# Optimization experiments

Hardware: AMD Instinct MI355X
Metric: run time of the kernel (lower is better)

## Reference

```python
import jax, jax.numpy as jnp
import numpy as np

B, S, E = 2, 2048, 2048
H, KV, D = 16, 4, 128
G = H // KV  # query heads per kv head
THETA = 10000.0


def setup_inputs() -> dict:
    key = jax.random.key(0)
    ks = jax.random.split(key, 5)
    scale = 0.02
    return {
        "x": jax.random.normal(ks[0], (B, S, E), dtype=jnp.float32),
        "Wq": jax.random.normal(ks[1], (E, H * D), dtype=jnp.float32) * scale,
        "Wk": jax.random.normal(ks[2], (E, KV * D), dtype=jnp.float32) * scale,
        "Wv": jax.random.normal(ks[3], (E, KV * D), dtype=jnp.float32) * scale,
        "Wo": jax.random.normal(ks[4], (E, E), dtype=jnp.float32) * scale,
    }


def _rope_tables(seq_len, head_dim, theta):
    inv_freq = 1.0 / theta ** (jnp.arange(0, head_dim, 2, dtype=jnp.float32) / head_dim)
    t = jnp.arange(seq_len, dtype=jnp.float32)
    freqs = jnp.outer(t, inv_freq)  # [S, D/2]
    cos = jnp.concatenate([jnp.cos(freqs), jnp.cos(freqs)], axis=-1)  # [S, D]
    sin = jnp.concatenate([jnp.sin(freqs), jnp.sin(freqs)], axis=-1)
    return cos, sin


def _apply_rope(x, cos, sin):
    # x: [B, h, S, D]; cos/sin: [S, D] broadcast over batch/heads
    d2 = x.shape[-1] // 2
    x1, x2 = x[..., :d2], x[..., d2:]
    rotated = jnp.concatenate([-x2, x1], axis=-1)
    return x * cos + rotated * sin


def reference(x, Wq, Wk, Wv, Wo):
    b, s, _ = x.shape
    q = (x @ Wq).reshape(b, s, H, D).transpose(0, 2, 1, 3)   # [B,H,S,D]
    k = (x @ Wk).reshape(b, s, KV, D).transpose(0, 2, 1, 3)  # [B,KV,S,D]
    v = (x @ Wv).reshape(b, s, KV, D).transpose(0, 2, 1, 3)

    cos, sin = _rope_tables(s, D, THETA)
    q = _apply_rope(q, cos, sin)
    k = _apply_rope(k, cos, sin)

    # GQA: q head h attends to kv head h // G (repeat_interleave order)
    qg = q.reshape(b, KV, G, s, D)
    scores = jnp.einsum("bkgsd,bktd->bkgst", qg, k) / jnp.sqrt(jnp.asarray(D, x.dtype))
    causal = jnp.tril(jnp.ones((s, s), dtype=bool))
    scores = jnp.where(causal, scores, jnp.asarray(-jnp.inf, scores.dtype))
    attn = jax.nn.softmax(scores, axis=-1)
    out = jnp.einsum("bkgst,bktd->bkgsd", attn, v)  # [B,KV,G,S,D]
    out = out.reshape(b, H, s, D).transpose(0, 2, 1, 3).reshape(b, s, H * D)
    return out @ Wo
```

## Files before the change

### kernel.cpp

```cpp
#include <hip/hip_runtime.h>
#include <stdint.h>

#define B_ 2
#define S_ 2048
#define E_ 2048
#define H_ 16
#define KV_ 4
#define D_ 128
#define G_ (H_ / KV_)
#define M_ (B_ * S_)

typedef unsigned short u16;
typedef unsigned int u32;
typedef __bf16 bf16x8 __attribute__((ext_vector_type(8)));
typedef float f32x4 __attribute__((ext_vector_type(4)));

__device__ __forceinline__ u16 f2bf(float f) {
  __bf16 h = (__bf16)f;
  return *(u16*)&h;
}
__device__ __forceinline__ float bf2f(u16 x) {
  return __uint_as_float(((u32)x) << 16);
}
__device__ __forceinline__ void store_c(u16* p, float v) { *p = f2bf(v); }
__device__ __forceinline__ void store_c(float* p, float v) { *p = v; }

__device__ __forceinline__ void gload_lds16(const u16* g, u16* lds) {
  __builtin_amdgcn_global_load_lds((const __attribute__((address_space(1))) u32*)g,
                                   (__attribute__((address_space(3))) u32*)lds,
                                   16, 0, 0);
}

__global__ __launch_bounds__(256) void convert_fp32_bf16(const float4* __restrict__ x,
                                                         uint2* __restrict__ o, int n4) {
  int i = blockIdx.x * 256 + threadIdx.x;
  if (i >= n4) return;
  float4 v = x[i];
  uint2 r;
  r.x = (u32)f2bf(v.x) | ((u32)f2bf(v.y) << 16);
  r.y = (u32)f2bf(v.z) | ((u32)f2bf(v.w) << 16);
  o[i] = r;
}

__global__ __launch_bounds__(256) void transpose_conv_w(const float* __restrict__ W,
                                                        u16* __restrict__ Wt,
                                                        int Kdim, int Ndim) {
  __shared__ float tile[32][33];
  int n0 = blockIdx.x * 32, k0 = blockIdx.y * 32;
  int tx = threadIdx.x, ty = threadIdx.y;
#pragma unroll
  for (int i = 0; i < 4; i++) {
    int r = ty + i * 8;
    tile[r][tx] = W[(size_t)(k0 + r) * Ndim + n0 + tx];
  }
  __syncthreads();
#pragma unroll
  for (int i = 0; i < 4; i++) {
    int r = ty + i * 8;
    Wt[(size_t)(n0 + r) * Kdim + k0 + tx] = f2bf(tile[tx][r]);
  }
}

__global__ __launch_bounds__(256) void transpose_v(const u16* __restrict__ V,
                                                   u16* __restrict__ Vt) {
  __shared__ u16 tile[32][33];
  int bkv = blockIdx.z;
  int b = bkv / KV_, kv = bkv % KV_;
  int s0 = blockIdx.x * 32, d0 = blockIdx.y * 32;
  int tx = threadIdx.x, ty = threadIdx.y;
#pragma unroll
  for (int i = 0; i < 4; i++) {
    int r = ty + i * 8;
    tile[r][tx] = V[((size_t)((b * S_ + s0 + r) * KV_ + kv)) * D_ + d0 + tx];
  }
  __syncthreads();
#pragma unroll
  for (int i = 0; i < 4; i++) {
    int r = ty + i * 8;
    Vt[((size_t)(b * KV_ + kv) * D_ + d0 + r) * S_ + s0 + tx] = tile[tx][r];
  }
}

__global__ __launch_bounds__(256) void rope_k_repack(const u16* __restrict__ Kin,
                                                     u16* __restrict__ Kp, int total) {
  int idx = blockIdx.x * 256 + threadIdx.x;
  if (idx >= total) return;
  int d = idx & 63;
  int rem = idx >> 6;
  int kv = rem % KV_;
  int row = rem / KV_;
  int b = row >> 11;
  int spos = row & (S_ - 1);
  size_t src = ((size_t)row * KV_ + kv) * D_ + d;
  float x0 = bf2f(Kin[src]);
  float x1 = bf2f(Kin[src + 64]);
  float ang = (float)spos * expf(-0.14391156831212787f * (float)d);
  float sn, cs;
  sincosf(ang, &sn, &cs);
  size_t dst = ((size_t)((b * KV_ + kv) * S_ + spos)) * D_ + d;
  Kp[dst]      = f2bf(x0 * cs - x1 * sn);
  Kp[dst + 64] = f2bf(x1 * cs + x0 * sn);
}

__global__ __launch_bounds__(256) void rope_q_inplace(u16* __restrict__ Qb, int total) {
  int idx = blockIdx.x * 256 + threadIdx.x;
  if (idx >= total) return;
  int d = idx & 63;
  int rem = idx >> 6;
  int h = rem & (H_ - 1);
  int row = rem >> 4;
  int spos = row & (S_ - 1);
  size_t base = ((size_t)row * H_ + h) * D_ + d;
  float x0 = bf2f(Qb[base]);
  float x1 = bf2f(Qb[base + 64]);
  float ang = (float)spos * expf(-0.14391156831212787f * (float)d);
  float sn, cs;
  sincosf(ang, &sn, &cs);
  const float scale = 0.08838834764831845f;
  Qb[base]      = f2bf((x0 * cs - x1 * sn) * scale);
  Qb[base + 64] = f2bf((x1 * cs + x0 * sn) * scale);
}

template <typename CT>
__device__ __forceinline__ void gemm256_body(const u16* __restrict__ A,
                                             const u16* __restrict__ Bt,
                                             CT* __restrict__ C,
                                             int Kdim, int Ndim, int m0, int n0) {
  extern __shared__ __align__(16) u16 smem[];
  const int tid  = threadIdx.x;
  const int lane = tid & 63;
  const int wave = tid >> 6;
  const int wm   = wave >> 2;
  const int wn   = wave & 3;
  const int bh   = wn >> 1;
  const int nb   = (wn & 1) * 64;
  const int quad = lane >> 4, lm = lane & 15;

  int soff[2], sldb[2];
#pragma unroll
  for (int i = 0; i < 2; i++) {
    int cc  = i * 512 + tid;
    int row = cc >> 3;
    int q   = (cc & 7) ^ (row & 7);
    soff[i] = row * Kdim + q * 8;
    sldb[i] = (i * 512 + wave * 64) * 8;
  }
  auto STAGE = [&](const u16* g, u16* l) {
    gload_lds16(g + soff[0], l + sldb[0]);
    gload_lds16(g + soff[1], l + sldb[1]);
  };

  int cs0 = ((0 + quad) ^ (lm & 7)) * 8;
  int cs1 = ((4 + quad) ^ (lm & 7)) * 8;

  const u16* Ag = A  + (size_t)m0 * Kdim;
  const u16* Bg = Bt + (size_t)n0 * Kdim;
  const size_t hstep = (size_t)128 * Kdim;

  f32x4 acc[8][4];
  f32x4 zero = {0.f, 0.f, 0.f, 0.f};
#pragma unroll
  for (int m = 0; m < 8; m++)
#pragma unroll
    for (int n = 0; n < 4; n++) acc[m][n] = zero;

  const int NKT = Kdim >> 6;

  STAGE(Bg,             smem + 32768 + 0 * 8192);
  STAGE(Ag,             smem + 0 * 8192);
  STAGE(Ag + hstep,     smem + 1 * 8192);
  STAGE(Bg + hstep,     smem + 32768 + 1 * 8192);
  STAGE(Bg + 64,        smem + 32768 + 2 * 8192);
  STAGE(Ag + 64,        smem + 2 * 8192);
  STAGE(Ag + hstep + 64, smem + 3 * 8192);
  asm volatile("s_waitcnt vmcnt(6)" ::: "memory");
  __builtin_amdgcn_s_barrier();

  for (int kt = 0; kt < NKT; ++kt) {
    const int cur = kt & 1;
    const u16* regA = smem + (cur * 2 + wm) * 8192;
    const u16* regB = smem + 32768 + (cur * 2 + bh) * 8192;
    bf16x8 af[4][2], bf[4][2];

#pragma unroll
    for (int n = 0; n < 4; n++) {
      bf[n][0] = *(const bf16x8*)(regB + (nb + n * 16 + lm) * 64 + cs0);
      bf[n][1] = *(const bf16x8*)(regB + (nb + n * 16 + lm) * 64 + cs1);
    }
#pragma unroll
    for (int m = 0; m < 4; m++) {
      af[m][0] = *(const bf16x8*)(regA + (m * 16 + lm) * 64 + cs0);
      af[m][1] = *(const bf16x8*)(regA + (m * 16 + lm) * 64 + cs1);
    }
    if (kt + 1 < NKT)
      STAGE(Bg + hstep + (size_t)(kt + 1) * 64,
            smem + 32768 + (((kt + 1) & 1) * 2 + 1) * 8192);
    asm volatile("s_waitcnt lgkmcnt(0)" ::: "memory");
    __builtin_amdgcn_s_barrier();
    __builtin_amdgcn_s_setprio(1);
#pragma unroll
    for (int m = 0; m < 4; m++)
#pragma unroll
      for (int n = 0; n < 2; n++) {
        acc[m][n] = __builtin_amdgcn_mfma_f32_16x16x32_bf16(af[m][0], bf[n][0], acc[m][n], 0, 0, 0);
        acc[m][n] = __builtin_amdgcn_mfma_f32_16x16x32_bf16(af[m][1], bf[n][1], acc[m][n], 0, 0, 0);
      }
    __builtin_amdgcn_s_setprio(0);
    __builtin_amdgcn_s_barrier();

    if (kt + 2 < NKT)
      STAGE(Bg + (size_t)(kt + 2) * 64, smem + 32768 + (cur * 2 + 0) * 8192);
    __builtin_amdgcn_s_barrier();
    __builtin_amdgcn_s_setprio(1);
#pragma unroll
    for (int m = 0; m < 4; m++)
#pragma unroll
      for (int n = 2; n < 4; n++) {
        acc[m][n] = __builtin_amdgcn_mfma_f32_16x16x32_bf16(af[m][0], bf[n][0], acc[m][n], 0, 0, 0);
        acc[m][n] = __builtin_amdgcn_mfma_f32_16x16x32_bf16(af[m][1], bf[n][1], acc[m][n], 0, 0, 0);
      }
    __builtin_amdgcn_s_setprio(0);
    __builtin_amdgcn_s_barrier();

#pragma unroll
    for (int m = 0; m < 4; m++) {
      af[m][0] = *(const bf16x8*)(regA + ((m + 4) * 16 + lm) * 64 + cs0);
      af[m][1] = *(const bf16x8*)(regA + ((m + 4) * 16 + lm) * 64 + cs1);
    }
    asm volatile("s_waitcnt lgkmcnt(0)" ::: "memory");
    __builtin_amdgcn_s_barrier();
    __builtin_amdgcn_s_setprio(1);
#pragma unroll
    for (int m = 0; m < 4; m++)
#pragma unroll
      for (int n = 0; n < 2; n++) {
        acc[m + 4][n] = __builtin_amdgcn_mfma_f32_16x16x32_bf16(af[m][0], bf[n][0], acc[m + 4][n], 0, 0, 0);
        acc[m + 4][n] = __builtin_amdgcn_mfma_f32_16x16x32_bf16(af[m][1], bf[n][1], acc[m + 4][n], 0, 0, 0);
      }
    __builtin_amdgcn_s_setprio(0);
    __builtin_amdgcn_s_barrier();

    if (kt + 2 < NKT) {
      STAGE(Ag + (size_t)(kt + 2) * 64,         smem + (cur * 2 + 0) * 8192);
      STAGE(Ag + hstep + (size_t)(kt + 2) * 64, smem + (cur * 2 + 1) * 8192);
    }
    __builtin_amdgcn_s_setprio(1);
#pragma unroll
    for (int m = 0; m < 4; m++)
#pragma unroll
      for (int n = 2; n < 4; n++) {
        acc[m + 4][n] = __builtin_amdgcn_mfma_f32_16x16x32_bf16(af[m][0], bf[n][0], acc[m + 4][n], 0, 0, 0);
        acc[m + 4][n] = __builtin_amdgcn_mfma_f32_16x16x32_bf16(af[m][1], bf[n][1], acc[m + 4][n], 0, 0, 0);
      }
    __builtin_amdgcn_s_setprio(0);
    asm volatile("s_waitcnt vmcnt(6)" ::: "memory");
    __builtin_amdgcn_s_barrier();
  }

#pragma unroll
  for (int m = 0; m < 8; m++) {
    const int row = m0 + wm * 128 + m * 16 + quad * 4;
#pragma unroll
    for (int n = 0; n < 4; n++) {
      const int col = n0 + wn * 64 + n * 16 + lm;
#pragma unroll
      for (int r = 0; r < 4; r++)
        store_c(C + (size_t)(row + r) * Ndim + col, acc[m][n][r]);
    }
  }
}

__global__ __launch_bounds__(512, 2) void gemm256_qkv(const u16* __restrict__ A,
                                                      const u16* __restrict__ WqT,
                                                      const u16* __restrict__ WkT,
                                                      const u16* __restrict__ WvT,
                                                      u16* __restrict__ Qb,
                                                      u16* __restrict__ Kb,
                                                      u16* __restrict__ Vb) {
  int bx = blockIdx.x;
  const u16* Bt;
  u16* C;
  int n0, Ndim;
  if (bx < 8)       { Bt = WqT; C = Qb; n0 = bx * 256;        Ndim = 2048; }
  else if (bx < 10) { Bt = WkT; C = Kb; n0 = (bx - 8) * 256;  Ndim = 512; }
  else              { Bt = WvT; C = Vb; n0 = (bx - 10) * 256; Ndim = 512; }
  gemm256_body<u16>(A, Bt, C, 2048, Ndim, blockIdx.y * 256, n0);
}

__global__ __launch_bounds__(512, 2) void gemm256x128_wo(const u16* __restrict__ A,
                                                         const u16* __restrict__ Bt,
                                                         float* __restrict__ C) {
  extern __shared__ __align__(16) u16 smem[];
  const int Kdim = 2048, Ndim = 2048;
  const int m0 = blockIdx.y * 256, n0 = blockIdx.x * 128;
  const int tid  = threadIdx.x;
  const int lane = tid & 63;
  const int wave = tid >> 6;
  const int wm   = wave >> 2;
  const int wn   = wave & 3;
  const int bh   = wn >> 1;
  const int nb   = (wn & 1) * 32;
  const int quad = lane >> 4, lm = lane & 15;

  int soffA[2], sldbA[2];
#pragma unroll
  for (int i = 0; i < 2; i++) {
    int cc  = i * 512 + tid;
    int row = cc >> 3;
    int q   = (cc & 7) ^ (row & 7);
    soffA[i] = row * Kdim + q * 8;
    sldbA[i] = (i * 512 + wave * 64) * 8;
  }
  const int rowB = tid >> 3;
  const int soffB = rowB * Kdim + (((tid & 7) ^ (rowB & 7)) * 8);
  const int sldbB = wave * 512;
  auto STAGE_A = [&](const u16* g, u16* l) {
    gload_lds16(g + soffA[0], l + sldbA[0]);
    gload_lds16(g + soffA[1], l + sldbA[1]);
  };
  auto STAGE_B = [&](const u16* g, u16* l) {
    gload_lds16(g + soffB, l + sldbB);
  };

  int cs0 = ((0 + quad) ^ (lm & 7)) * 8;
  int cs1 = ((4 + quad) ^ (lm & 7)) * 8;

  const u16* Ag = A  + (size_t)m0 * Kdim;
  const u16* Bg = Bt + (size_t)n0 * Kdim;
  const size_t hstepA = (size_t)128 * Kdim;
  const size_t hstepB = (size_t)64 * Kdim;

  f32x4 acc[8][2];
  f32x4 zero = {0.f, 0.f, 0.f, 0.f};
#pragma unroll
  for (int m = 0; m < 8; m++) {
    acc[m][0] = zero;
    acc[m][1] = zero;
  }

  const int NKT = Kdim >> 6;

  STAGE_B(Bg,              smem + 32768 + 0 * 4096);
  STAGE_A(Ag,              smem + 0 * 8192);
  STAGE_A(Ag + hstepA,     smem + 1 * 8192);
  STAGE_B(Bg + hstepB,     smem + 32768 + 1 * 4096);
  STAGE_B(Bg + 64,         smem + 32768 + 2 * 4096);
  STAGE_A(Ag + 64,         smem + 2 * 8192);
  STAGE_A(Ag + hstepA + 64, smem + 3 * 8192);
  asm volatile("s_waitcnt vmcnt(5)" ::: "memory");
  __builtin_amdgcn_s_barrier();

  for (int kt = 0; kt < NKT; ++kt) {
    const int cur = kt & 1;
    const u16* regA = smem + (cur * 2 + wm) * 8192;
    const u16* regB = smem + 32768 + (cur * 2 + bh) * 4096;
    bf16x8 af[4][2], bf[2][2];

#pragma unroll
    for (int n = 0; n < 2; n++) {
      bf[n][0] = *(const bf16x8*)(regB + (nb + n * 16 + lm) * 64 + cs0);
      bf[n][1] = *(const bf16x8*)(regB + (nb + n * 16 + lm) * 64 + cs1);
    }
#pragma unroll
    for (int m = 0; m < 4; m++) {
      af[m][0] = *(const bf16x8*)(regA + (m * 16 + lm) * 64 + cs0);
      af[m][1] = *(const bf16x8*)(regA + (m * 16 + lm) * 64 + cs1);
    }
    if (kt + 1 < NKT)
      STAGE_B(Bg + hstepB + (size_t)(kt + 1) * 64,
              smem + 32768 + (((kt + 1) & 1) * 2 + 1) * 4096);
    asm volatile("s_waitcnt lgkmcnt(0)" ::: "memory");
    __builtin_amdgcn_s_barrier();
    __builtin_amdgcn_s_setprio(1);
#pragma unroll
    for (int m = 0; m < 2; m++)
#pragma unroll
      for (int n = 0; n < 2; n++) {
        acc[m][n] = __builtin_amdgcn_mfma_f32_16x16x32_bf16(af[m][0], bf[n][0], acc[m][n], 0, 0, 0);
        acc[m][n] = __builtin_amdgcn_mfma_f32_16x16x32_bf16(af[m][1], bf[n][1], acc[m][n], 0, 0, 0);
      }
    __builtin_amdgcn_s_setprio(0);
    __builtin_amdgcn_s_barrier();

    if (kt + 2 < NKT)
      STAGE_B(Bg + (size_t)(kt + 2) * 64, smem + 32768 + (cur * 2 + 0) * 4096);
    __builtin_amdgcn_s_barrier();
    __builtin_amdgcn_s_setprio(1);
#pragma unroll
    for (int m = 2; m < 4; m++)
#pragma unroll
      for (int n = 0; n < 2; n++) {
        acc[m][n] = __builtin_amdgcn_mfma_f32_16x16x32_bf16(af[m][0], bf[n][0], acc[m][n], 0, 0, 0);
        acc[m][n] = __builtin_amdgcn_mfma_f32_16x16x32_bf16(af[m][1], bf[n][1], acc[m][n], 0, 0, 0);
      }
    __builtin_amdgcn_s_setprio(0);
    __builtin_amdgcn_s_barrier();

#pragma unroll
    for (int m = 0; m < 4; m++) {
      af[m][0] = *(const bf16x8*)(regA + ((m + 4) * 16 + lm) * 64 + cs0);
      af[m][1] = *(const bf16x8*)(regA + ((m + 4) * 16 + lm) * 64 + cs1);
    }
    asm volatile("s_waitcnt lgkmcnt(0)" ::: "memory");
    __builtin_amdgcn_s_barrier();
    __builtin_amdgcn_s_setprio(1);
#pragma unroll
    for (int m = 0; m < 2; m++)
#pragma unroll
      for (int n = 0; n < 2; n++) {
        acc[m + 4][n] = __builtin_amdgcn_mfma_f32_16x16x32_bf16(af[m][0], bf[n][0], acc[m + 4][n], 0, 0, 0);
        acc[m + 4][n] = __builtin_amdgcn_mfma_f32_16x16x32_bf16(af[m][1], bf[n][1], acc[m + 4][n], 0, 0, 0);
      }
    __builtin_amdgcn_s_setprio(0);
    __builtin_amdgcn_s_barrier();

    if (kt + 2 < NKT) {
      STAGE_A(Ag + (size_t)(kt + 2) * 64,          smem + (cur * 2 + 0) * 8192);
      STAGE_A(Ag + hstepA + (size_t)(kt + 2) * 64, smem + (cur * 2 + 1) * 8192);
    }
    __builtin_amdgcn_s_setprio(1);
#pragma unroll
    for (int m = 2; m < 4; m++)
#pragma unroll
      for (int n = 0; n < 2; n++) {
        acc[m + 4][n] = __builtin_amdgcn_mfma_f32_16x16x32_bf16(af[m][0], bf[n][0], acc[m + 4][n], 0, 0, 0);
        acc[m + 4][n] = __builtin_amdgcn_mfma_f32_16x16x32_bf16(af[m][1], bf[n][1], acc[m + 4][n], 0, 0, 0);
      }
    __builtin_amdgcn_s_setprio(0);
    asm volatile("s_waitcnt vmcnt(5)" ::: "memory");
    __builtin_amdgcn_s_barrier();
  }

#pragma unroll
  for (int m = 0; m < 8; m++) {
    const int row = m0 + wm * 128 + m * 16 + quad * 4;
#pragma unroll
    for (int n = 0; n < 2; n++) {
      const int col = n0 + wn * 32 + n * 16 + lm;
#pragma unroll
      for (int r = 0; r < 4; r++)
        C[(size_t)(row + r) * Ndim + col] = acc[m][n][r];
    }
  }
}

__global__ __launch_bounds__(256, 2) void attn_kernel(const u16* __restrict__ Q,
                                                      const u16* __restrict__ Kp,
                                                      const u16* __restrict__ Vt,
                                                      u16* __restrict__ O) {
  __shared__ __align__(16) u16 Ksh[2][64 * 128];
  __shared__ __align__(16) u16 Vsh[2][128 * 64];
  __shared__ __align__(16) u16 Psh[4][16 * 64];

  const int tid = threadIdx.x;
  const int lane = tid & 63;
  const int wave = tid >> 6;
  const int quad = lane >> 4, lm = lane & 15;
  const int b = blockIdx.z, h = blockIdx.x;
  const int kh = h / G_;

  const u16* Kbase = Kp + (size_t)(b * KV_ + kh) * S_ * D_;
  const u16* Vbase = Vt + (size_t)(b * KV_ + kh) * D_ * S_;
  u16* pw = &Psh[wave][0];

  int offK[4], offV[4], ldsOff[4];
#pragma unroll
  for (int i = 0; i < 4; i++) {
    int idx = (wave * 4 + i) * 64 + lane;
    int rK = idx >> 4;
    int cK = (idx & 15) ^ (rK & 7);
    offK[i] = rK * 128 + cK * 8;
    int rV = idx >> 3;
    int cV = (idx & 7) ^ (rV & 7);
    offV[i] = rV * S_ + cV * 8;
    ldsOff[i] = (wave * 4 + i) * 512;
  }

  bf16x8 onesb;
#pragma unroll
  for (int j = 0; j < 8; j++) onesb[j] = (__bf16)1.0f;

#pragma unroll
  for (int half = 0; half < 2; half++) {
    const int qi = half ? blockIdx.y : (31 - blockIdx.y);
    const int sq0 = qi * 64;
    const int nT = qi + 1;
    const int wrow = sq0 + wave * 16;

    const u16* qptr = Q + ((size_t)(b * S_ + wrow + lm) * H_ + h) * D_;
    bf16x8 qf[4];
#pragma unroll
    for (int ks = 0; ks < 4; ks++)
      qf[ks] = *(const bf16x8*)(qptr + ks * 32 + quad * 8);

    f32x4 o[8];
    f32x4 lacc = {0.f, 0.f, 0.f, 0.f};
#pragma unroll
    for (int i = 0; i < 8; i++) o[i] = f32x4{0.f, 0.f, 0.f, 0.f};

    __syncthreads();

#pragma unroll
    for (int i = 0; i < 4; i++)
      gload_lds16(Kbase + offK[i], &Ksh[0][ldsOff[i]]);
#pragma unroll
    for (int i = 0; i < 4; i++)
      gload_lds16(Vbase + offV[i], &Vsh[0][ldsOff[i]]);

    for (int t = 0; t < nT; t++) {
      const int sk0 = t << 6;

      __builtin_amdgcn_s_barrier();

      if (t + 1 < nT) {
        const u16* kg = Kbase + (size_t)(t + 1) * 64 * 128;
        const u16* vg = Vbase + (t + 1) * 64;
        u16* kb_next = &Ksh[(t + 1) & 1][0];
        u16* vb_next = &Vsh[(t + 1) & 1][0];
#pragma unroll
        for (int i = 0; i < 4; i++)
          gload_lds16(kg + offK[i], kb_next + ldsOff[i]);
#pragma unroll
        for (int i = 0; i < 4; i++)
          gload_lds16(vg + offV[i], vb_next + ldsOff[i]);
        asm volatile("s_waitcnt vmcnt(8)" ::: "memory");
      } else {
        asm volatile("s_waitcnt vmcnt(0)" ::: "memory");
      }

      __builtin_amdgcn_s_barrier();
      __builtin_amdgcn_sched_barrier(0);

      const u16* kbuf = &Ksh[t & 1][0];
      f32x4 sc[4];
#pragma unroll
      for (int nt = 0; nt < 4; nt++) sc[nt] = f32x4{0.f, 0.f, 0.f, 0.f};
      __builtin_amdgcn_s_setprio(1);
#pragma unroll
      for (int ks = 0; ks < 4; ks++) {
#pragma unroll
        for (int nt = 0; nt < 4; nt++) {
          int R = nt * 16 + lm;
          bf16x8 kb = *(const bf16x8*)(kbuf + R * 128 + (((ks * 4 + quad) ^ (R & 7)) * 8));
          sc[nt] = __builtin_amdgcn_mfma_f32_16x16x32_bf16(qf[ks], kb, sc[nt], 0, 0, 0);
        }
      }
      __builtin_amdgcn_s_setprio(0);
      const bool nm = (sk0 + 63 > wrow);
#pragma unroll
      for (int nt = 0; nt < 4; nt++)
#pragma unroll
        for (int r = 0; r < 4; r++) {
          float p = __expf(sc[nt][r]);
          if (nm) {
            int kc = sk0 + nt * 16 + lm;
            int qr = wrow + quad * 4 + r;
            p = (kc > qr) ? 0.f : p;
          }
          sc[nt][r] = p;
        }
#pragma unroll
      for (int nt = 0; nt < 4; nt++)
#pragma unroll
        for (int r = 0; r < 4; r++) {
          int p = quad * 4 + r;
          int c = nt * 2 + (lm >> 3);
          pw[p * 64 + ((c ^ (p & 7)) * 8) + (lm & 7)] = f2bf(sc[nt][r]);
        }
      const u16* vbuf = &Vsh[t & 1][0];
      __builtin_amdgcn_s_setprio(1);
#pragma unroll
      for (int ks = 0; ks < 2; ks++) {
        int pr = lm;
        bf16x8 pa = *(const bf16x8*)(pw + pr * 64 + (((ks * 4 + quad) ^ (pr & 7)) * 8));
        lacc = __builtin_amdgcn_mfma_f32_16x16x32_bf16(pa, onesb, lacc, 0, 0, 0);
#pragma unroll
        for (int d8 = 0; d8 < 8; d8++) {
          int R = d8 * 16 + lm;
          bf16x8 vb = *(const bf16x8*)(vbuf + R * 64 + (((ks * 4 + quad) ^ (R & 7)) * 8));
          o[d8] = __builtin_amdgcn_mfma_f32_16x16x32_bf16(pa, vb, o[d8], 0, 0, 0);
        }
      }
      __builtin_amdgcn_s_setprio(0);
    }

    float inv[4];
#pragma unroll
    for (int r = 0; r < 4; r++) inv[r] = 1.0f / lacc[r];
#pragma unroll
    for (int d8 = 0; d8 < 8; d8++)
#pragma unroll
      for (int r = 0; r < 4; r++) {
        int srow = wrow + quad * 4 + r;
        O[((size_t)(b * S_ + srow) * H_ + h) * D_ + d8 * 16 + lm] = f2bf(o[d8][r] * inv[r]);
      }
  }
}

extern "C" void kernel_launch(void* const* d_in, const int* in_sizes, int n_in,
                              void* d_out, int out_size, void* d_ws, size_t ws_size,
                              hipStream_t stream) {
  const float* x  = (const float*)d_in[0];
  const float* Wq = (const float*)d_in[1];
  const float* Wk = (const float*)d_in[2];
  const float* Wv = (const float*)d_in[3];
  const float* Wo = (const float*)d_in[4];
  float* out = (float*)d_out;
  char* ws = (char*)d_ws;
  u16* Xb  = (u16*)(ws);
  u16* WqT = (u16*)(ws + (16ull << 20));
  u16* WkT = (u16*)(ws + (24ull << 20));
  u16* WvT = (u16*)(ws + (26ull << 20));
  u16* WoT = (u16*)(ws + (28ull << 20));
  u16* Qb  = (u16*)(ws + (36ull << 20));
  u16* Kb  = (u16*)(ws + (52ull << 20));
  u16* Vb  = (u16*)(ws + (56ull << 20));
  u16* Vt  = (u16*)(ws + (60ull << 20));
  u16* Ob  = (u16*)(ws + (64ull << 20));
  u16* Kp  = (u16*)(ws + (80ull << 20));

  static bool attr_set = false;
  if (!attr_set) {
    hipFuncSetAttribute((const void*)gemm256_qkv,
                        hipFuncAttributeMaxDynamicSharedMemorySize, 131072);
    hipFuncSetAttribute((const void*)gemm256x128_wo,
                        hipFuncAttributeMaxDynamicSharedMemorySize, 98304);
    attr_set = true;
  }

  dim3 tb32(32, 8);

  convert_fp32_bf16<<<dim3(M_ * E_ / 4 / 256), 256, 0, stream>>>((const float4*)x, (uint2*)Xb, M_ * E_ / 4);
  transpose_conv_w<<<dim3(2048 / 32, 2048 / 32), tb32, 0, stream>>>(Wq, WqT, E_, H_ * D_);
  transpose_conv_w<<<dim3(512 / 32, 2048 / 32), tb32, 0, stream>>>(Wk, WkT, E_, KV_ * D_);
  transpose_conv_w<<<dim3(512 / 32, 2048 / 32), tb32, 0, stream>>>(Wv, WvT, E_, KV_ * D_);
  transpose_conv_w<<<dim3(2048 / 32, 2048 / 32), tb32, 0, stream>>>(Wo, WoT, E_, E_);

  gemm256_qkv<<<dim3(12, M_ / 256), 512, 131072, stream>>>(Xb, WqT, WkT, WvT, Qb, Kb, Vb);

  rope_q_inplace<<<dim3(M_ * H_ * 64 / 256), 256, 0, stream>>>(Qb, M_ * H_ * 64);

  rope_k_repack<<<dim3(M_ * KV_ * 64 / 256), 256, 0, stream>>>(Kb, Kp, M_ * KV_ * 64);

  transpose_v<<<dim3(S_ / 32, D_ / 32, B_ * KV_), tb32, 0, stream>>>(Vb, Vt);

  attn_kernel<<<dim3(H_, 16, B_), 256, 0, stream>>>(Qb, Kp, Vt, Ob);

  gemm256x128_wo<<<dim3(2048 / 128, M_ / 256), 512, 98304, stream>>>(Ob, WoT, out);
}
```

Baseline: 297.9 us.

## Fuse QKV projection into one 256x192-tile GEMM with interleaved QKV output

Replaces the three-way dispatched 256x256 QKV GEMM with a single GEMM over the concatenated transposed weights (contiguous in workspace). It uses 256x192 tiles, giving a 16x16 grid instead of 12x16, and writes one interleaved [M, 3072] QKV buffer that rope, the V transpose and attention read through strided indexing. It also merges the four weight transpose launches into one and precomputes a cos/sin table so the rope kernels no longer evaluate sincos per element. The intent is a grid that fills the GPU's compute units better and fewer launches, at the cost of a narrower N tile with less reuse per block and strided row accesses in the downstream kernels.

Measured after the change: 288.2 us. -3.2%, faster.

```diff
diff --git a/kernel.cpp b/kernel.cpp
--- a/kernel.cpp
+++ b/kernel.cpp
@@ -9,6 +9,7 @@
 #define D_ 128
 #define G_ (H_ / KV_)
 #define M_ (B_ * S_)
+#define NQKV 3072
 
 typedef unsigned short u16;
 typedef unsigned int u32;
@@ -29,6 +30,16 @@
   __builtin_amdgcn_global_load_lds((const __attribute__((address_space(1))) u32*)g,
                                    (__attribute__((address_space(3))) u32*)lds,
                                    16, 0, 0);
+}
+
+__global__ __launch_bounds__(256) void build_trig(float2* __restrict__ tbl) {
+  int i = blockIdx.x * 256 + threadIdx.x;
+  if (i >= S_ * 64) return;
+  int d = i & 63, s = i >> 6;
+  float ang = (float)s * expf(-0.14391156831212787f * (float)d);
+  float sn, cs;
+  sincosf(ang, &sn, &cs);
+  tbl[i] = make_float2(cs, sn);
 }
 
 __global__ __launch_bounds__(256) void convert_fp32_bf16(const float4* __restrict__ x,
@@ -42,11 +53,24 @@
   o[i] = r;
 }
 
-__global__ __launch_bounds__(256) void transpose_conv_w(const float* __restrict__ W,
-                                                        u16* __restrict__ Wt,
-                                                        int Kdim, int Ndim) {
+__global__ __launch_bounds__(256) void transpose_conv_all(const float* __restrict__ Wq,
+                                                          const float* __restrict__ Wk,
+                                                          const float* __restrict__ Wv,
+                                                          const float* __restrict__ Wo,
+                                                          u16* __restrict__ WqT,
+                                                          u16* __restrict__ WkT,
+                                                          u16* __restrict__ WvT,
+                                                          u16* __restrict__ WoT) {
   __shared__ float tile[32][33];
-  int n0 = blockIdx.x * 32, k0 = blockIdx.y * 32;
+  int bx = blockIdx.x;
+  const float* W;
+  u16* Wt;
+  int Ndim, nx;
+  if (bx < 64)       { W = Wq; Wt = WqT; Ndim = 2048; nx = bx; }
+  else if (bx < 80)  { W = Wk; Wt = WkT; Ndim = 512;  nx = bx - 64; }
+  else if (bx < 96)  { W = Wv; Wt = WvT; Ndim = 512;  nx = bx - 80; }
+  else               { W = Wo; Wt = WoT; Ndim = 2048; nx = bx - 96; }
+  int n0 = nx * 32, k0 = blockIdx.y * 32;
   int tx = threadIdx.x, ty = threadIdx.y;
 #pragma unroll
   for (int i = 0; i < 4; i++) {
@@ -57,11 +81,11 @@
 #pragma unroll
   for (int i = 0; i < 4; i++) {
     int r = ty + i * 8;
-    Wt[(size_t)(n0 + r) * Kdim + k0 + tx] = f2bf(tile[tx][r]);
-  }
-}
-
-__global__ __launch_bounds__(256) void transpose_v(const u16* __restrict__ V,
+    Wt[(size_t)(n0 + r) * 2048 + k0 + tx] = f2bf(tile[tx][r]);
+  }
+}
+
+__global__ __launch_bounds__(256) void transpose_v(const u16* __restrict__ QKV,
                                                    u16* __restrict__ Vt) {
   __shared__ u16 tile[32][33];
   int bkv = blockIdx.z;
@@ -71,7 +95,7 @@
 #pragma unroll
   for (int i = 0; i < 4; i++) {
     int r = ty + i * 8;
-    tile[r][tx] = V[((size_t)((b * S_ + s0 + r) * KV_ + kv)) * D_ + d0 + tx];
+    tile[r][tx] = QKV[(size_t)(b * S_ + s0 + r) * NQKV + 2560 + kv * D_ + d0 + tx];
   }
   __syncthreads();
 #pragma unroll
@@ -81,28 +105,30 @@
   }
 }
 
-__global__ __launch_bounds__(256) void rope_k_repack(const u16* __restrict__ Kin,
-                                                     u16* __restrict__ Kp, int total) {
+__global__ __launch_bounds__(256) void rope_k_repack(const u16* __restrict__ QKV,
+                                                     u16* __restrict__ Kp,
+                                                     const float2* __restrict__ tbl,
+                                                     int total) {
   int idx = blockIdx.x * 256 + threadIdx.x;
   if (idx >= total) return;
   int d = idx & 63;
   int rem = idx >> 6;
-  int kv = rem % KV_;
-  int row = rem / KV_;
+  int kv = rem & (KV_ - 1);
+  int row = rem >> 2;
   int b = row >> 11;
   int spos = row & (S_ - 1);
-  size_t src = ((size_t)row * KV_ + kv) * D_ + d;
-  float x0 = bf2f(Kin[src]);
-  float x1 = bf2f(Kin[src + 64]);
-  float ang = (float)spos * expf(-0.14391156831212787f * (float)d);
-  float sn, cs;
-  sincosf(ang, &sn, &cs);
+  size_t src = (size_t)row * NQKV + 2048 + kv * D_ + d;
+  float x0 = bf2f(QKV[src]);
+  float x1 = bf2f(QKV[src + 64]);
+  float2 t = tbl[(spos << 6) + d];
   size_t dst = ((size_t)((b * KV_ + kv) * S_ + spos)) * D_ + d;
-  Kp[dst]      = f2bf(x0 * cs - x1 * sn);
-  Kp[dst + 64] = f2bf(x1 * cs + x0 * sn);
-}
-
-__global__ __launch_bounds__(256) void rope_q_inplace(u16* __restrict__ Qb, int total) {
+  Kp[dst]      = f2bf(x0 * t.x - x1 * t.y);
+  Kp[dst + 64] = f2bf(x1 * t.x + x0 * t.y);
+}
+
+__global__ __launch_bounds__(256) void rope_q_inplace(u16* __restrict__ QKV,
+                                                      const float2* __restrict__ tbl,
+                                                      int total) {
   int idx = blockIdx.x * 256 + threadIdx.x;
   if (idx >= total) return;
   int d = idx & 63;
@@ -110,44 +136,46 @@
   int h = rem & (H_ - 1);
   int row = rem >> 4;
   int spos = row & (S_ - 1);
-  size_t base = ((size_t)row * H_ + h) * D_ + d;
-  float x0 = bf2f(Qb[base]);
-  float x1 = bf2f(Qb[base + 64]);
-  float ang = (float)spos * expf(-0.14391156831212787f * (float)d);
-  float sn, cs;
-  sincosf(ang, &sn, &cs);
+  size_t base = (size_t)row * NQKV + h * D_ + d;
+  float x0 = bf2f(QKV[base]);
+  float x1 = bf2f(QKV[base + 64]);
+  float2 t = tbl[(spos << 6) + d];
   const float scale = 0.08838834764831845f;
-  Qb[base]      = f2bf((x0 * cs - x1 * sn) * scale);
-  Qb[base + 64] = f2bf((x1 * cs + x0 * sn) * scale);
-}
-
-template <typename CT>
-__device__ __forceinline__ void gemm256_body(const u16* __restrict__ A,
-                                             const u16* __restrict__ Bt,
-                                             CT* __restrict__ C,
-                                             int Kdim, int Ndim, int m0, int n0) {
+  QKV[base]      = f2bf((x0 * t.x - x1 * t.y) * scale);
+  QKV[base + 64] = f2bf((x1 * t.x + x0 * t.y) * scale);
+}
+
+__global__ __launch_bounds__(512, 2) void gemm256x192_qkv(const u16* __restrict__ A,
+                                                          const u16* __restrict__ Bt,
+                                                          u16* __restrict__ C) {
   extern __shared__ __align__(16) u16 smem[];
+  const int Kdim = 2048;
+  const int m0 = blockIdx.y * 256, n0 = blockIdx.x * 192;
   const int tid  = threadIdx.x;
   const int lane = tid & 63;
   const int wave = tid >> 6;
   const int wm   = wave >> 2;
   const int wn   = wave & 3;
-  const int bh   = wn >> 1;
-  const int nb   = (wn & 1) * 64;
   const int quad = lane >> 4, lm = lane & 15;
 
-  int soff[2], sldb[2];
+  int soffA[2], sldbA[2];
 #pragma unroll
   for (int i = 0; i < 2; i++) {
     int cc  = i * 512 + tid;
     int row = cc >> 3;
     int q   = (cc & 7) ^ (row & 7);
-    soff[i] = row * Kdim + q * 8;
-    sldb[i] = (i * 512 + wave * 64) * 8;
-  }
-  auto STAGE = [&](const u16* g, u16* l) {
-    gload_lds16(g + soff[0], l + sldb[0]);
-    gload_lds16(g + soff[1], l + sldb[1]);
+    soffA[i] = row * Kdim + q * 8;
+    sldbA[i] = (i * 512 + wave * 64) * 8;
+  }
+  const int rowB = tid >> 3;
+  const int soffB = rowB * Kdim + (((tid & 7) ^ (rowB & 7)) * 8);
+  const int sldbB = wave * 512;
+  auto STAGE_A = [&](const u16* g, u16* l) {
+    gload_lds16(g + soffA[0], l + sldbA[0]);
+    gload_lds16(g + soffA[1], l + sldbA[1]);
+  };
+  auto STAGE_B = [&](const u16* g, u16* l) {
+    gload_lds16(g + soffB, l + sldbB);
   };
 
   int cs0 = ((0 + quad) ^ (lm & 7)) * 8;
@@ -155,46 +183,60 @@
 
   const u16* Ag = A  + (size_t)m0 * Kdim;
   const u16* Bg = Bt + (size_t)n0 * Kdim;
-  const size_t hstep = (size_t)128 * Kdim;
-
-  f32x4 acc[8][4];
+  const size_t hstepA = (size_t)128 * Kdim;
+  const size_t tstepB = (size_t)64 * Kdim;
+
+  f32x4 acc[8][3];
   f32x4 zero = {0.f, 0.f, 0.f, 0.f};
 #pragma unroll
   for (int m = 0; m < 8; m++)
 #pragma unroll
-    for (int n = 0; n < 4; n++) acc[m][n] = zero;
+    for (int n = 0; n < 3; n++) acc[m][n] = zero;
+
+  int bthird[3], brow[3];
+#pragma unroll
+  for (int nt = 0; nt < 3; nt++) {
+    int R = wn * 48 + nt * 16;
+    bthird[nt] = R >> 6;
+    brow[nt] = (R & 63) + lm;
+  }
 
   const int NKT = Kdim >> 6;
 
-  STAGE(Bg,             smem + 32768 + 0 * 8192);
-  STAGE(Ag,             smem + 0 * 8192);
-  STAGE(Ag + hstep,     smem + 1 * 8192);
-  STAGE(Bg + hstep,     smem + 32768 + 1 * 8192);
-  STAGE(Bg + 64,        smem + 32768 + 2 * 8192);
-  STAGE(Ag + 64,        smem + 2 * 8192);
-  STAGE(Ag + hstep + 64, smem + 3 * 8192);
-  asm volatile("s_waitcnt vmcnt(6)" ::: "memory");
+  STAGE_B(Bg,                    smem + 32768 + 0 * 4096);
+  STAGE_A(Ag,                    smem + 0 * 8192);
+  STAGE_A(Ag + hstepA,           smem + 1 * 8192);
+  STAGE_B(Bg + tstepB,           smem + 32768 + 1 * 4096);
+  STAGE_B(Bg + 2 * tstepB,       smem + 32768 + 2 * 4096);
+  STAGE_B(Bg + 64,               smem + 32768 + 3 * 4096);
+  STAGE_A(Ag + 64,               smem + 2 * 8192);
+  STAGE_A(Ag + hstepA + 64,      smem + 3 * 8192);
+  asm volatile("s_waitcnt vmcnt(5)" ::: "memory");
   __builtin_amdgcn_s_barrier();
 
   for (int kt = 0; kt < NKT; ++kt) {
     const int cur = kt & 1;
-    const u16* regA = smem + (cur * 2 + wm) * 8192;
-    const u16* regB = smem + 32768 + (cur * 2 + bh) * 8192;
-    bf16x8 af[4][2], bf[4][2];
-
-#pragma unroll
-    for (int n = 0; n < 4; n++) {
-      bf[n][0] = *(const bf16x8*)(regB + (nb + n * 16 + lm) * 64 + cs0);
-      bf[n][1] = *(const bf16x8*)(regB + (nb + n * 16 + lm) * 64 + cs1);
+    const u16* regA  = smem + (cur * 2 + wm) * 8192;
+    const u16* regB3 = smem + 32768 + cur * 3 * 4096;
+    bf16x8 af[4][2], bf[3][2];
+
+#pragma unroll
+    for (int nt = 0; nt < 3; nt++) {
+      const u16* p = regB3 + bthird[nt] * 4096 + brow[nt] * 64;
+      bf[nt][0] = *(const bf16x8*)(p + cs0);
+      bf[nt][1] = *(const bf16x8*)(p + cs1);
     }
 #pragma unroll
     for (int m = 0; m < 4; m++) {
       af[m][0] = *(const bf16x8*)(regA + (m * 16 + lm) * 64 + cs0);
       af[m][1] = *(const bf16x8*)(regA + (m * 16 + lm) * 64 + cs1);
     }
-    if (kt + 1 < NKT)
-      STAGE(Bg + hstep + (size_t)(kt + 1) * 64,
-            smem + 32768 + (((kt + 1) & 1) * 2 + 1) * 8192);
+    if (kt + 1 < NKT) {
+      const u16* bn = Bg + (size_t)(kt + 1) * 64;
+      u16* sb = smem + 32768 + ((cur ^ 1) * 3) * 4096;
+      STAGE_B(bn + tstepB,     sb + 1 * 4096);
+      STAGE_B(bn + 2 * tstepB, sb + 2 * 4096);
+    }
     asm volatile("s_waitcnt lgkmcnt(0)" ::: "memory");
     __builtin_amdgcn_s_barrier();
     __builtin_amdgcn_s_setprio(1);
@@ -209,16 +251,14 @@
     __builtin_amdgcn_s_barrier();
 
     if (kt + 2 < NKT)
-      STAGE(Bg + (size_t)(kt + 2) * 64, smem + 32768 + (cur * 2 + 0) * 8192);
-    __builtin_amdgcn_s_barrier();
-    __builtin_amdgcn_s_setprio(1);
-#pragma unroll
-    for (int m = 0; m < 4; m++)
-#pragma unroll
-      for (int n = 2; n < 4; n++) {
-        acc[m][n] = __builtin_amdgcn_mfma_f32_16x16x32_bf16(af[m][0], bf[n][0], acc[m][n], 0, 0, 0);
-        acc[m][n] = __builtin_amdgcn_mfma_f32_16x16x32_bf16(af[m][1], bf[n][1], acc[m][n], 0, 0, 0);
-      }
+      STAGE_B(Bg + (size_t)(kt + 2) * 64, smem + 32768 + (cur * 3 + 0) * 4096);
+    __builtin_amdgcn_s_barrier();
+    __builtin_amdgcn_s_setprio(1);
+#pragma unroll
+    for (int m = 0; m < 4; m++) {
+      acc[m][2] = __builtin_amdgcn_mfma_f32_16x16x32_bf16(af[m][0], bf[2][0], acc[m][2], 0, 0, 0);
+      acc[m][2] = __builtin_amdgcn_mfma_f32_16x16x32_bf16(af[m][1], bf[2][1], acc[m][2], 0, 0, 0);
+    }
     __builtin_amdgcn_s_setprio(0);
     __builtin_amdgcn_s_barrier();
 
@@ -241,19 +281,17 @@
     __builtin_amdgcn_s_barrier();
 
     if (kt + 2 < NKT) {
-      STAGE(Ag + (size_t)(kt + 2) * 64,         smem + (cur * 2 + 0) * 8192);
-      STAGE(Ag + hstep + (size_t)(kt + 2) * 64, smem + (cur * 2 + 1) * 8192);
-    }
-    __builtin_amdgcn_s_setprio(1);
-#pragma unroll
-    for (int m = 0; m < 4; m++)
-#pragma unroll
-      for (int n = 2; n < 4; n++) {
-        acc[m + 4][n] = __builtin_amdgcn_mfma_f32_16x16x32_bf16(af[m][0], bf[n][0], acc[m + 4][n], 0, 0, 0);
-        acc[m + 4][n] = __builtin_amdgcn_mfma_f32_16x16x32_bf16(af[m][1], bf[n][1], acc[m + 4][n], 0, 0, 0);
-      }
-    __builtin_amdgcn_s_setprio(0);
-    asm volatile("s_waitcnt vmcnt(6)" ::: "memory");
+      STAGE_A(Ag + (size_t)(kt + 2) * 64,          smem + (cur * 2 + 0) * 8192);
+      STAGE_A(Ag + hstepA + (size_t)(kt + 2) * 64, smem + (cur * 2 + 1) * 8192);
+    }
+    __builtin_amdgcn_s_setprio(1);
+#pragma unroll
+    for (int m = 0; m < 4; m++) {
+      acc[m + 4][2] = __builtin_amdgcn_mfma_f32_16x16x32_bf16(af[m][0], bf[2][0], acc[m + 4][2], 0, 0, 0);
+      acc[m + 4][2] = __builtin_amdgcn_mfma_f32_16x16x32_bf16(af[m][1], bf[2][1], acc[m + 4][2], 0, 0, 0);
+    }
+    __builtin_amdgcn_s_setprio(0);
+    asm volatile("s_waitcnt vmcnt(5)" ::: "memory");
     __builtin_amdgcn_s_barrier();
   }
 
@@ -261,30 +299,13 @@
   for (int m = 0; m < 8; m++) {
     const int row = m0 + wm * 128 + m * 16 + quad * 4;
 #pragma unroll
-    for (int n = 0; n < 4; n++) {
-      const int col = n0 + wn * 64 + n * 16 + lm;
+    for (int n = 0; n < 3; n++) {
+      const int col = n0 + wn * 48 + n * 16 + lm;
 #pragma unroll
       for (int r = 0; r < 4; r++)
-        store_c(C + (size_t)(row + r) * Ndim + col, acc[m][n][r]);
-    }
-  }
-}
-
-__global__ __launch_bounds__(512, 2) void gemm256_qkv(const u16* __restrict__ A,
-                                                      const u16* __restrict__ WqT,
-                                                      const u16* __restrict__ WkT,
-                                                      const u16* __restrict__ WvT,
-                                                      u16* __restrict__ Qb,
-                                                      u16* __restrict__ Kb,
-                                                      u16* __restrict__ Vb) {
-  int bx = blockIdx.x;
-  const u16* Bt;
-  u16* C;
-  int n0, Ndim;
-  if (bx < 8)       { Bt = WqT; C = Qb; n0 = bx * 256;        Ndim = 2048; }
-  else if (bx < 10) { Bt = WkT; C = Kb; n0 = (bx - 8) * 256;  Ndim = 512; }
-  else              { Bt = WvT; C = Vb; n0 = (bx - 10) * 256; Ndim = 512; }
-  gemm256_body<u16>(A, Bt, C, 2048, Ndim, blockIdx.y * 256, n0);
+        C[(size_t)(row + r) * NQKV + col] = f2bf(acc[m][n][r]);
+    }
+  }
 }
 
 __global__ __launch_bounds__(512, 2) void gemm256x128_wo(const u16* __restrict__ A,
@@ -487,7 +508,7 @@
     const int nT = qi + 1;
     const int wrow = sq0 + wave * 16;
 
-    const u16* qptr = Q + ((size_t)(b * S_ + wrow + lm) * H_ + h) * D_;
+    const u16* qptr = Q + (size_t)(b * S_ + wrow + lm) * NQKV + h * D_;
     bf16x8 qf[4];
 #pragma unroll
     for (int ks = 0; ks < 4; ks++)
@@ -607,22 +628,22 @@
   const float* Wo = (const float*)d_in[4];
   float* out = (float*)d_out;
   char* ws = (char*)d_ws;
-  u16* Xb  = (u16*)(ws);
-  u16* WqT = (u16*)(ws + (16ull << 20));
-  u16* WkT = (u16*)(ws + (24ull << 20));
-  u16* WvT = (u16*)(ws + (26ull << 20));
-  u16* WoT = (u16*)(ws + (28ull << 20));
-  u16* Qb  = (u16*)(ws + (36ull << 20));
-  u16* Kb  = (u16*)(ws + (52ull << 20));
-  u16* Vb  = (u16*)(ws + (56ull << 20));
-  u16* Vt  = (u16*)(ws + (60ull << 20));
-  u16* Ob  = (u16*)(ws + (64ull << 20));
-  u16* Kp  = (u16*)(ws + (80ull << 20));
+  u16* Xb   = (u16*)(ws);
+  u16* Wcat = (u16*)(ws + (16ull << 20));
+  u16* WqT  = Wcat;
+  u16* WkT  = (u16*)(ws + (24ull << 20));
+  u16* WvT  = (u16*)(ws + (26ull << 20));
+  u16* WoT  = (u16*)(ws + (28ull << 20));
+  u16* QKVb = (u16*)(ws + (36ull << 20));
+  u16* Vt   = (u16*)(ws + (60ull << 20));
+  u16* Ob   = (u16*)(ws + (64ull << 20));
+  u16* Kp   = (u16*)(ws + (80ull << 20));
+  float2* trig = (float2*)(ws + (84ull << 20));
 
   static bool attr_set = false;
   if (!attr_set) {
-    hipFuncSetAttribute((const void*)gemm256_qkv,
-                        hipFuncAttributeMaxDynamicSharedMemorySize, 131072);
+    hipFuncSetAttribute((const void*)gemm256x192_qkv,
+                        hipFuncAttributeMaxDynamicSharedMemorySize, 114688);
     hipFuncSetAttribute((const void*)gemm256x128_wo,
                         hipFuncAttributeMaxDynamicSharedMemorySize, 98304);
     attr_set = true;
@@ -630,21 +651,21 @@
 
   dim3 tb32(32, 8);
 
+  build_trig<<<dim3(S_ * 64 / 256), 256, 0, stream>>>(trig);
+
   convert_fp32_bf16<<<dim3(M_ * E_ / 4 / 256), 256, 0, stream>>>((const float4*)x, (uint2*)Xb, M_ * E_ / 4);
-  transpose_conv_w<<<dim3(2048 / 32, 2048 / 32), tb32, 0, stream>>>(Wq, WqT, E_, H_ * D_);
-  transpose_conv_w<<<dim3(512 / 32, 2048 / 32), tb32, 0, stream>>>(Wk, WkT, E_, KV_ * D_);
-  transpose_conv_w<<<dim3(512 / 32, 2048 / 32), tb32, 0, stream>>>(Wv, WvT, E_, KV_ * D_);
-  transpose_conv_w<<<dim3(2048 / 32, 2048 / 32), tb32, 0, stream>>>(Wo, WoT, E_, E_);
-
-  gemm256_qkv<<<dim3(12, M_ / 256), 512, 131072, stream>>>(Xb, WqT, WkT, WvT, Qb, Kb, Vb);
-
-  rope_q_inplace<<<dim3(M_ * H_ * 64 / 256), 256, 0, stream>>>(Qb, M_ * H_ * 64);
-
-  rope_k_repack<<<dim3(M_ * KV_ * 64 / 256), 256, 0, stream>>>(Kb, Kp, M_ * KV_ * 64);
-
-  transpose_v<<<dim3(S_ / 32, D_ / 32, B_ * KV_), tb32, 0, stream>>>(Vb, Vt);
-
-  attn_kernel<<<dim3(H_, 16, B_), 256, 0, stream>>>(Qb, Kp, Vt, Ob);
+
+  transpose_conv_all<<<dim3(160, 64), tb32, 0, stream>>>(Wq, Wk, Wv, Wo, WqT, WkT, WvT, WoT);
+
+  gemm256x192_qkv<<<dim3(16, 16), 512, 114688, stream>>>(Xb, Wcat, QKVb);
+
+  rope_q_inplace<<<dim3(M_ * H_ * 64 / 256), 256, 0, stream>>>(QKVb, trig, M_ * H_ * 64);
+
+  rope_k_repack<<<dim3(M_ * KV_ * 64 / 256), 256, 0, stream>>>(QKVb, Kp, trig, M_ * KV_ * 64);
+
+  transpose_v<<<dim3(S_ / 32, D_ / 32, B_ * KV_), tb32, 0, stream>>>(QKVb, Vt);
+
+  attn_kernel<<<dim3(H_, 16, B_), 256, 0, stream>>>(QKVb, Kp, Vt, Ob);
 
   gemm256x128_wo<<<dim3(2048 / 128, M_ / 256), 512, 98304, stream>>>(Ob, WoT, out);
 }
```
